# Optimization experiments

Measured on AMD Instinct MI355X. Metric: run time of the kernel, lower is better.

The kernel has to match this reference:

```python
import jax, jax.numpy as jnp
import numpy as np

B, H, S, DH = 2, 16, 2048, 64
MASK_FILL = -10000.0


def setup_inputs() -> dict:
    key = jax.random.key(0)
    kq, kk, kv = jax.random.split(key, 3)
    q = jax.random.normal(kq, (B, H, S, DH), dtype=jnp.float32)
    k = jax.random.normal(kk, (B, H, S, DH), dtype=jnp.float32)
    v = jax.random.normal(kv, (B, H, S, DH), dtype=jnp.float32)
    # causal mask: True where attention is disallowed (upper triangle)
    mask = jnp.triu(jnp.ones((S, S), dtype=jnp.bool_), k=1)
    return {"q": q, "k": k, "v": v, "mask": mask}


def reference(q, k, v, mask):
    scale = 1.0 / jnp.sqrt(jnp.asarray(k.shape[-1], dtype=q.dtype))
    # scores: [B, H, S_q, S_k]
    scores = jnp.einsum("bhqd,bhkd->bhqk", q, k) * scale
    # additive mask: masked_fill on a zeros [S_k, S_v] matrix -> -10000 where mask
    attn_bias = jnp.where(mask, jnp.asarray(MASK_FILL, dtype=k.dtype),
                          jnp.asarray(0.0, dtype=k.dtype))
    scores = scores + attn_bias  # broadcast over batch/heads
    attn = jax.nn.softmax(scores, axis=-1)
    # dropout_rate = 0.0 -> identity
    return jnp.einsum("bhqk,bhkd->bhqd", attn, v)
```

## Files before the change

### kernel.cpp

```cpp
#include <hip/hip_runtime.h>


#define S_LEN  2048
#define DHDIM  64
#define NHEADS 32
#define LDP    72
#define M2     23.083120654223414f
#define QSCALE 0.18033688011117658f

#if __has_builtin(__builtin_amdgcn_exp2f)
#define EXP2(x) __builtin_amdgcn_exp2f(x)
#else
#define EXP2(x) exp2f(x)
#endif

typedef __attribute__((ext_vector_type(8))) short bf16x8;
typedef __attribute__((ext_vector_type(4))) float f32x4;

__device__ __forceinline__ unsigned short f2bf(float f) {
    unsigned u = __float_as_uint(f);
    return (unsigned short)((u + 0x7fffu + ((u >> 16) & 1u)) >> 16);
}
__device__ __forceinline__ void ld8(const float* p, float* f) {
    float4 a = *(const float4*)p, b = *(const float4*)(p + 4);
    f[0]=a.x; f[1]=a.y; f[2]=a.z; f[3]=a.w; f[4]=b.x; f[5]=b.y; f[6]=b.z; f[7]=b.w;
}
__device__ __forceinline__ uint4 pack8(const float* f, float scale) {
    union { uint4 v; unsigned short s[8]; } w;
    #pragma unroll
    for (int j = 0; j < 8; j++) w.s[j] = f2bf(f[j] * scale);
    return w.v;
}

__global__ __launch_bounds__(256) void conv_qk(
    const float* __restrict__ Qf, const float* __restrict__ Kf,
    unsigned short* __restrict__ qb, unsigned short* __restrict__ kb)
{
    size_t off = ((size_t)blockIdx.x * 256 + threadIdx.x) * 8;
    float f[8];
    ld8(Qf + off, f); *(uint4*)(qb + off) = pack8(f, QSCALE);
    ld8(Kf + off, f); *(uint4*)(kb + off) = pack8(f, 1.0f);
}

__global__ __launch_bounds__(256) void trans_v(
    const float* __restrict__ Vf, unsigned short* __restrict__ vtb)
{
    __shared__ unsigned short lt[64][LDP];
    const int st = blockIdx.x, bh = blockIdx.y;
    const float* vp = Vf + ((size_t)bh * S_LEN + st * 64) * DHDIM;
    for (int c = threadIdx.x; c < 512; c += 256) {
        int s = c >> 3, d0 = (c & 7) * 8;
        float f[8]; ld8(vp + s * DHDIM + d0, f);
        #pragma unroll
        for (int j = 0; j < 8; j++) lt[d0 + j][s] = f2bf(f[j]);
    }
    __syncthreads();
    unsigned short* op = vtb + (size_t)bh * DHDIM * S_LEN + st * 64;
    for (int c = threadIdx.x; c < 512; c += 256) {
        int d = c >> 3, s0 = (c & 7) * 8;
        *(uint4*)(op + (size_t)d * S_LEN + s0) = *(const uint4*)&lt[d][s0];
    }
}

template <bool PRE>
__global__ __launch_bounds__(256) void fattn_kernel(
    const void* __restrict__ Qp, const void* __restrict__ Kp,
    const void* __restrict__ Vp, float* __restrict__ O)
{
    __shared__ unsigned short qs[64][LDP];
    __shared__ unsigned short ks[64][LDP];
    __shared__ unsigned short vts[80][LDP];
    __shared__ unsigned short ps[4][16][LDP];

    const int bh = blockIdx.y, tid = threadIdx.x;
    const int wave = tid >> 6, lane = tid & 63;
    const int quad = lane >> 4, l16 = lane & 15;
    const int qrow = wave * 16 + quad * 4;

    for (int i = tid; i < 16 * LDP; i += 256) {
        int r = i / LDP, c = i % LDP;
        vts[64 + r][c] = (r == 0 && c < 64) ? (unsigned short)0x3F80 : (unsigned short)0;
    }

    #pragma unroll 1
    for (int half = 0; half < 2; half++) {
        const int qt = half ? 31 - blockIdx.x : blockIdx.x;
        __syncthreads();

        if constexpr (PRE) {
            const unsigned short* src = (const unsigned short*)Qp
                + ((size_t)bh * S_LEN + qt * 64) * DHDIM;
            for (int c = tid; c < 512; c += 256) {
                int row = c >> 3, c8 = (c & 7) * 8;
                *(uint4*)&qs[row][c8] = *(const uint4*)(src + row * DHDIM + c8);
            }
        } else {
            const float* src = (const float*)Qp + ((size_t)bh * S_LEN + qt * 64) * DHDIM;
            for (int c = tid; c < 512; c += 256) {
                int row = c >> 3, c8 = (c & 7) * 8;
                float f[8]; ld8(src + row * DHDIM + c8, f);
                *(uint4*)&qs[row][c8] = pack8(f, QSCALE);
            }
        }

        f32x4 of[5];
        #pragma unroll
        for (int n = 0; n < 5; n++) of[n] = (f32x4){0.f, 0.f, 0.f, 0.f};

        for (int kt = 0; kt <= qt; kt++) {
            __syncthreads();
            if constexpr (PRE) {
                const unsigned short* ksrc = (const unsigned short*)Kp
                    + ((size_t)bh * S_LEN + kt * 64) * DHDIM;
                const unsigned short* vsrc = (const unsigned short*)Vp
                    + (size_t)bh * DHDIM * S_LEN + kt * 64;
                for (int c = tid; c < 512; c += 256) {
                    int row = c >> 3, c8 = (c & 7) * 8;
                    *(uint4*)&ks[row][c8]  = *(const uint4*)(ksrc + row * DHDIM + c8);
                    *(uint4*)&vts[row][c8] = *(const uint4*)(vsrc + (size_t)row * S_LEN + c8);
                }
            } else {
                const float* ksrc = (const float*)Kp + ((size_t)bh * S_LEN + kt * 64) * DHDIM;
                const float* vsrc = (const float*)Vp + ((size_t)bh * S_LEN + kt * 64) * DHDIM;
                for (int c = tid; c < 512; c += 256) {
                    int row = c >> 3, c8 = (c & 7) * 8;
                    float f[8];
                    ld8(ksrc + row * DHDIM + c8, f);
                    *(uint4*)&ks[row][c8] = pack8(f, 1.0f);
                    ld8(vsrc + row * DHDIM + c8, f);
                    #pragma unroll
                    for (int j = 0; j < 8; j++) vts[c8 + j][row] = f2bf(f[j]);
                }
            }
            __syncthreads();

            bf16x8 aq0 = *(const bf16x8*)&qs[wave * 16 + l16][quad * 8];
            bf16x8 aq1 = *(const bf16x8*)&qs[wave * 16 + l16][32 + quad * 8];
            f32x4 sf[4];
            #pragma unroll
            for (int n = 0; n < 4; n++) {
                bf16x8 b0 = *(const bf16x8*)&ks[n * 16 + l16][quad * 8];
                bf16x8 b1 = *(const bf16x8*)&ks[n * 16 + l16][32 + quad * 8];
                sf[n] = (f32x4){0.f, 0.f, 0.f, 0.f};
                sf[n] = __builtin_amdgcn_mfma_f32_16x16x32_bf16(aq0, b0, sf[n], 0, 0, 0);
                sf[n] = __builtin_amdgcn_mfma_f32_16x16x32_bf16(aq1, b1, sf[n], 0, 0, 0);
            }

            const bool diag = (kt == qt);
            #pragma unroll
            for (int n = 0; n < 4; n++) {
                int col = n * 16 + l16;
                #pragma unroll
                for (int r = 0; r < 4; r++) {
                    float t = fminf(sf[n][r] - M2, 80.f);
                    float p = EXP2(t);
                    if (diag && col > qrow + r) p = 0.f;
                    ps[wave][quad * 4 + r][col] = (unsigned short)(__float_as_uint(p) >> 16);
                }
            }
            asm volatile("s_waitcnt lgkmcnt(0)" ::: "memory");

            bf16x8 ap0 = *(const bf16x8*)&ps[wave][l16][quad * 8];
            bf16x8 ap1 = *(const bf16x8*)&ps[wave][l16][32 + quad * 8];
            #pragma unroll
            for (int n = 0; n < 5; n++) {
                bf16x8 bv0 = *(const bf16x8*)&vts[n * 16 + l16][quad * 8];
                bf16x8 bv1 = *(const bf16x8*)&vts[n * 16 + l16][32 + quad * 8];
                of[n] = __builtin_amdgcn_mfma_f32_16x16x32_bf16(ap0, bv0, of[n], 0, 0, 0);
                of[n] = __builtin_amdgcn_mfma_f32_16x16x32_bf16(ap1, bv1, of[n], 0, 0, 0);
            }
        }

        float* op = O + ((size_t)bh * S_LEN + qt * 64) * DHDIM;
        #pragma unroll
        for (int r = 0; r < 4; r++) {
            float l = __shfl(of[4][r], lane & 48, 64);
            float inv = 1.f / l;
            int row = qrow + r;
            #pragma unroll
            for (int n = 0; n < 4; n++)
                op[row * DHDIM + n * 16 + l16] = of[n][r] * inv;
        }
    }
}

extern "C" void kernel_launch(void* const* d_in, const int* in_sizes, int n_in,
                              void* d_out, int out_size, void* d_ws, size_t ws_size,
                              hipStream_t stream) {
    const float* Q = (const float*)d_in[0];
    const float* K = (const float*)d_in[1];
    const float* V = (const float*)d_in[2];
    float* O = (float*)d_out;
    const size_t N = (size_t)NHEADS * S_LEN * DHDIM;

    if (ws_size >= 3 * N * sizeof(unsigned short) && d_ws) {
        unsigned short* qb  = (unsigned short*)d_ws;
        unsigned short* kb  = qb + N;
        unsigned short* vtb = kb + N;
        conv_qk<<<(int)(N / (8 * 256)), 256, 0, stream>>>(Q, K, qb, kb);
        trans_v<<<dim3(S_LEN / 64, NHEADS), 256, 0, stream>>>(V, vtb);
        fattn_kernel<true><<<dim3(16, NHEADS), 256, 0, stream>>>(qb, kb, vtb, O);
    } else {
        fattn_kernel<false><<<dim3(16, NHEADS), 256, 0, stream>>>(Q, K, V, O);
    }
}
```

Measured before the change: 163.8 us.

## Fuse prep kernels, one q-tile per block, register row-sum instead of MFMA ones column

```diff
diff --git a/kernel.cpp b/kernel.cpp
--- a/kernel.cpp
+++ b/kernel.cpp
@@ -8,18 +8,15 @@
 #define M2     23.083120654223414f
 #define QSCALE 0.18033688011117658f
 
-#if __has_builtin(__builtin_amdgcn_exp2f)
-#define EXP2(x) __builtin_amdgcn_exp2f(x)
-#else
-#define EXP2(x) exp2f(x)
-#endif
-
 typedef __attribute__((ext_vector_type(8))) short bf16x8;
 typedef __attribute__((ext_vector_type(4))) float f32x4;
 
 __device__ __forceinline__ unsigned short f2bf(float f) {
     unsigned u = __float_as_uint(f);
     return (unsigned short)((u + 0x7fffu + ((u >> 16) & 1u)) >> 16);
+}
+__device__ __forceinline__ float bf2f(unsigned short b) {
+    return __uint_as_float(((unsigned)b) << 16);
 }
 __device__ __forceinline__ void ld8(const float* p, float* f) {
     float4 a = *(const float4*)p, b = *(const float4*)(p + 4);
@@ -32,21 +29,13 @@
     return w.v;
 }
 
-__global__ __launch_bounds__(256) void conv_qk(
+__global__ __launch_bounds__(256) void prep(
     const float* __restrict__ Qf, const float* __restrict__ Kf,
-    unsigned short* __restrict__ qb, unsigned short* __restrict__ kb)
+    const float* __restrict__ Vf, unsigned short* __restrict__ qb,
+    unsigned short* __restrict__ kb, unsigned short* __restrict__ vtb)
 {
-    size_t off = ((size_t)blockIdx.x * 256 + threadIdx.x) * 8;
-    float f[8];
-    ld8(Qf + off, f); *(uint4*)(qb + off) = pack8(f, QSCALE);
-    ld8(Kf + off, f); *(uint4*)(kb + off) = pack8(f, 1.0f);
-}
-
-__global__ __launch_bounds__(256) void trans_v(
-    const float* __restrict__ Vf, unsigned short* __restrict__ vtb)
-{
+    const int st = blockIdx.x, bh = blockIdx.y;
     __shared__ unsigned short lt[64][LDP];
-    const int st = blockIdx.x, bh = blockIdx.y;
     const float* vp = Vf + ((size_t)bh * S_LEN + st * 64) * DHDIM;
     for (int c = threadIdx.x; c < 512; c += 256) {
         int s = c >> 3, d0 = (c & 7) * 8;
@@ -54,6 +43,12 @@
         #pragma unroll
         for (int j = 0; j < 8; j++) lt[d0 + j][s] = f2bf(f[j]);
     }
+    size_t off = ((size_t)(bh * 32 + st) * 4096) + (size_t)threadIdx.x * 16;
+    float f[8];
+    ld8(Qf + off, f);     *(uint4*)(qb + off)     = pack8(f, QSCALE);
+    ld8(Qf + off + 8, f); *(uint4*)(qb + off + 8) = pack8(f, QSCALE);
+    ld8(Kf + off, f);     *(uint4*)(kb + off)     = pack8(f, 1.0f);
+    ld8(Kf + off + 8, f); *(uint4*)(kb + off + 8) = pack8(f, 1.0f);
     __syncthreads();
     unsigned short* op = vtb + (size_t)bh * DHDIM * S_LEN + st * 64;
     for (int c = threadIdx.x; c < 512; c += 256) {
@@ -69,118 +64,117 @@
 {
     __shared__ unsigned short qs[64][LDP];
     __shared__ unsigned short ks[64][LDP];
-    __shared__ unsigned short vts[80][LDP];
+    __shared__ unsigned short vts[64][LDP];
     __shared__ unsigned short ps[4][16][LDP];
 
+    const int qt = 31 - blockIdx.x;
     const int bh = blockIdx.y, tid = threadIdx.x;
     const int wave = tid >> 6, lane = tid & 63;
     const int quad = lane >> 4, l16 = lane & 15;
     const int qrow = wave * 16 + quad * 4;
 
-    for (int i = tid; i < 16 * LDP; i += 256) {
-        int r = i / LDP, c = i % LDP;
-        vts[64 + r][c] = (r == 0 && c < 64) ? (unsigned short)0x3F80 : (unsigned short)0;
+    if constexpr (PRE) {
+        const unsigned short* src = (const unsigned short*)Qp
+            + ((size_t)bh * S_LEN + qt * 64) * DHDIM;
+        for (int c = tid; c < 512; c += 256) {
+            int row = c >> 3, c8 = (c & 7) * 8;
+            *(uint4*)&qs[row][c8] = *(const uint4*)(src + row * DHDIM + c8);
+        }
+    } else {
+        const float* src = (const float*)Qp + ((size_t)bh * S_LEN + qt * 64) * DHDIM;
+        for (int c = tid; c < 512; c += 256) {
+            int row = c >> 3, c8 = (c & 7) * 8;
+            float f[8]; ld8(src + row * DHDIM + c8, f);
+            *(uint4*)&qs[row][c8] = pack8(f, QSCALE);
+        }
     }
 
-    #pragma unroll 1
-    for (int half = 0; half < 2; half++) {
-        const int qt = half ? 31 - blockIdx.x : blockIdx.x;
+    float l_p[4];
+    f32x4 of[4];
+    #pragma unroll
+    for (int r = 0; r < 4; r++) l_p[r] = 0.f;
+    #pragma unroll
+    for (int n = 0; n < 4; n++) of[n] = (f32x4){0.f, 0.f, 0.f, 0.f};
+
+    for (int kt = 0; kt <= qt; kt++) {
         __syncthreads();
 
         if constexpr (PRE) {
-            const unsigned short* src = (const unsigned short*)Qp
-                + ((size_t)bh * S_LEN + qt * 64) * DHDIM;
+            const unsigned short* ksrc = (const unsigned short*)Kp
+                + ((size_t)bh * S_LEN + kt * 64) * DHDIM;
+            const unsigned short* vsrc = (const unsigned short*)Vp
+                + (size_t)bh * DHDIM * S_LEN + kt * 64;
             for (int c = tid; c < 512; c += 256) {
                 int row = c >> 3, c8 = (c & 7) * 8;
-                *(uint4*)&qs[row][c8] = *(const uint4*)(src + row * DHDIM + c8);
+                *(uint4*)&ks[row][c8]  = *(const uint4*)(ksrc + row * DHDIM + c8);
+                *(uint4*)&vts[row][c8] = *(const uint4*)(vsrc + (size_t)row * S_LEN + c8);
             }
         } else {
-            const float* src = (const float*)Qp + ((size_t)bh * S_LEN + qt * 64) * DHDIM;
+            const float* ksrc = (const float*)Kp + ((size_t)bh * S_LEN + kt * 64) * DHDIM;
+            const float* vsrc = (const float*)Vp + ((size_t)bh * S_LEN + kt * 64) * DHDIM;
             for (int c = tid; c < 512; c += 256) {
                 int row = c >> 3, c8 = (c & 7) * 8;
-                float f[8]; ld8(src + row * DHDIM + c8, f);
-                *(uint4*)&qs[row][c8] = pack8(f, QSCALE);
+                float f[8];
+                ld8(ksrc + row * DHDIM + c8, f);
+                *(uint4*)&ks[row][c8] = pack8(f, 1.0f);
+                ld8(vsrc + row * DHDIM + c8, f);
+                #pragma unroll
+                for (int j = 0; j < 8; j++) vts[c8 + j][row] = f2bf(f[j]);
             }
         }
+        __syncthreads();
 
-        f32x4 of[5];
+        bf16x8 aq0 = *(const bf16x8*)&qs[wave * 16 + l16][quad * 8];
+        bf16x8 aq1 = *(const bf16x8*)&qs[wave * 16 + l16][32 + quad * 8];
+        f32x4 sf[4];
         #pragma unroll
-        for (int n = 0; n < 5; n++) of[n] = (f32x4){0.f, 0.f, 0.f, 0.f};
+        for (int n = 0; n < 4; n++) {
+            bf16x8 b0 = *(const bf16x8*)&ks[n * 16 + l16][quad * 8];
+            bf16x8 b1 = *(const bf16x8*)&ks[n * 16 + l16][32 + quad * 8];
+            sf[n] = (f32x4){0.f, 0.f, 0.f, 0.f};
+            sf[n] = __builtin_amdgcn_mfma_f32_16x16x32_bf16(aq0, b0, sf[n], 0, 0, 0);
+            sf[n] = __builtin_amdgcn_mfma_f32_16x16x32_bf16(aq1, b1, sf[n], 0, 0, 0);
+        }
 
-        for (int kt = 0; kt <= qt; kt++) {
-            __syncthreads();
-            if constexpr (PRE) {
-                const unsigned short* ksrc = (const unsigned short*)Kp
-                    + ((size_t)bh * S_LEN + kt * 64) * DHDIM;
-                const unsigned short* vsrc = (const unsigned short*)Vp
-                    + (size_t)bh * DHDIM * S_LEN + kt * 64;
-                for (int c = tid; c < 512; c += 256) {
-                    int row = c >> 3, c8 = (c & 7) * 8;
-                    *(uint4*)&ks[row][c8]  = *(const uint4*)(ksrc + row * DHDIM + c8);
-                    *(uint4*)&vts[row][c8] = *(const uint4*)(vsrc + (size_t)row * S_LEN + c8);
-                }
-            } else {
-                const float* ksrc = (const float*)Kp + ((size_t)bh * S_LEN + kt * 64) * DHDIM;
-                const float* vsrc = (const float*)Vp + ((size_t)bh * S_LEN + kt * 64) * DHDIM;
-                for (int c = tid; c < 512; c += 256) {
-                    int row = c >> 3, c8 = (c & 7) * 8;
-                    float f[8];
-                    ld8(ksrc + row * DHDIM + c8, f);
-                    *(uint4*)&ks[row][c8] = pack8(f, 1.0f);
-                    ld8(vsrc + row * DHDIM + c8, f);
-                    #pragma unroll
-                    for (int j = 0; j < 8; j++) vts[c8 + j][row] = f2bf(f[j]);
-                }
-            }
-            __syncthreads();
-
-            bf16x8 aq0 = *(const bf16x8*)&qs[wave * 16 + l16][quad * 8];
-            bf16x8 aq1 = *(const bf16x8*)&qs[wave * 16 + l16][32 + quad * 8];
-            f32x4 sf[4];
+        const bool diag = (kt == qt);
+        #pragma unroll
+        for (int n = 0; n < 4; n++) {
+            int col = n * 16 + l16;
             #pragma unroll
-            for (int n = 0; n < 4; n++) {
-                bf16x8 b0 = *(const bf16x8*)&ks[n * 16 + l16][quad * 8];
-                bf16x8 b1 = *(const bf16x8*)&ks[n * 16 + l16][32 + quad * 8];
-                sf[n] = (f32x4){0.f, 0.f, 0.f, 0.f};
-                sf[n] = __builtin_amdgcn_mfma_f32_16x16x32_bf16(aq0, b0, sf[n], 0, 0, 0);
-                sf[n] = __builtin_amdgcn_mfma_f32_16x16x32_bf16(aq1, b1, sf[n], 0, 0, 0);
-            }
-
-            const bool diag = (kt == qt);
-            #pragma unroll
-            for (int n = 0; n < 4; n++) {
-                int col = n * 16 + l16;
-                #pragma unroll
-                for (int r = 0; r < 4; r++) {
-                    float t = fminf(sf[n][r] - M2, 80.f);
-                    float p = EXP2(t);
-                    if (diag && col > qrow + r) p = 0.f;
-                    ps[wave][quad * 4 + r][col] = (unsigned short)(__float_as_uint(p) >> 16);
-                }
-            }
-            asm volatile("s_waitcnt lgkmcnt(0)" ::: "memory");
-
-            bf16x8 ap0 = *(const bf16x8*)&ps[wave][l16][quad * 8];
-            bf16x8 ap1 = *(const bf16x8*)&ps[wave][l16][32 + quad * 8];
-            #pragma unroll
-            for (int n = 0; n < 5; n++) {
-                bf16x8 bv0 = *(const bf16x8*)&vts[n * 16 + l16][quad * 8];
-                bf16x8 bv1 = *(const bf16x8*)&vts[n * 16 + l16][32 + quad * 8];
-                of[n] = __builtin_amdgcn_mfma_f32_16x16x32_bf16(ap0, bv0, of[n], 0, 0, 0);
-                of[n] = __builtin_amdgcn_mfma_f32_16x16x32_bf16(ap1, bv1, of[n], 0, 0, 0);
+            for (int r = 0; r < 4; r++) {
+                float p = exp2f(sf[n][r] - M2);
+                if (diag && col > qrow + r) p = 0.f;
+                unsigned short pb = (unsigned short)(__float_as_uint(p) >> 16);
+                l_p[r] += bf2f(pb);
+                ps[wave][quad * 4 + r][col] = pb;
             }
         }
+        asm volatile("s_waitcnt lgkmcnt(0)" ::: "memory");
 
-        float* op = O + ((size_t)bh * S_LEN + qt * 64) * DHDIM;
+        bf16x8 ap0 = *(const bf16x8*)&ps[wave][l16][quad * 8];
+        bf16x8 ap1 = *(const bf16x8*)&ps[wave][l16][32 + quad * 8];
         #pragma unroll
-        for (int r = 0; r < 4; r++) {
-            float l = __shfl(of[4][r], lane & 48, 64);
-            float inv = 1.f / l;
-            int row = qrow + r;
-            #pragma unroll
-            for (int n = 0; n < 4; n++)
-                op[row * DHDIM + n * 16 + l16] = of[n][r] * inv;
+        for (int n = 0; n < 4; n++) {
+            bf16x8 bv0 = *(const bf16x8*)&vts[n * 16 + l16][quad * 8];
+            bf16x8 bv1 = *(const bf16x8*)&vts[n * 16 + l16][32 + quad * 8];
+            of[n] = __builtin_amdgcn_mfma_f32_16x16x32_bf16(ap0, bv0, of[n], 0, 0, 0);
+            of[n] = __builtin_amdgcn_mfma_f32_16x16x32_bf16(ap1, bv1, of[n], 0, 0, 0);
         }
+    }
+
+    float* op = O + ((size_t)bh * S_LEN + qt * 64) * DHDIM;
+    #pragma unroll
+    for (int r = 0; r < 4; r++) {
+        float l = l_p[r];
+        l += __shfl_xor(l, 1);
+        l += __shfl_xor(l, 2);
+        l += __shfl_xor(l, 4);
+        l += __shfl_xor(l, 8);
+        float inv = 1.f / l;
+        int row = qrow + r;
+        #pragma unroll
+        for (int n = 0; n < 4; n++)
+            op[row * DHDIM + n * 16 + l16] = of[n][r] * inv;
     }
 }
 
@@ -197,10 +191,9 @@
         unsigned short* qb  = (unsigned short*)d_ws;
         unsigned short* kb  = qb + N;
         unsigned short* vtb = kb + N;
-        conv_qk<<<(int)(N / (8 * 256)), 256, 0, stream>>>(Q, K, qb, kb);
-        trans_v<<<dim3(S_LEN / 64, NHEADS), 256, 0, stream>>>(V, vtb);
-        fattn_kernel<true><<<dim3(16, NHEADS), 256, 0, stream>>>(qb, kb, vtb, O);
+        prep<<<dim3(S_LEN / 64, NHEADS), 256, 0, stream>>>(Q, K, V, qb, kb, vtb);
+        fattn_kernel<true><<<dim3(32, NHEADS), 256, 0, stream>>>(qb, kb, vtb, O);
     } else {
-        fattn_kernel<false><<<dim3(16, NHEADS), 256, 0, stream>>>(Q, K, V, O);
+        fattn_kernel<false><<<dim3(32, NHEADS), 256, 0, stream>>>(Q, K, V, O);
     }
 }
```

New measurement: 186.7 us. 1.14x slower.
